# Kernel tuning notes

Measured on AMD Instinct MI355X. Metric: run time of the kernel, lower is better.

The kernel has to match this reference:

```python
import jax, jax.numpy as jnp
import numpy as np

B, T, S, D, V = 8, 128, 400, 512, 50000
EPS_LN = 1e-6

def setup_inputs() -> dict:
    key = jax.random.key(0)
    ks = jax.random.split(key, 10)
    a = jax.random.uniform(ks[0], (B, T, S), dtype=jnp.float32)
    attn_weights = a / jnp.sum(a, axis=-1, keepdims=True)  # row-stochastic like softmax attention
    return {
        'x': jax.random.normal(ks[1], (B, T, D), dtype=jnp.float32),
        'x_t': jax.random.normal(ks[2], (B, T, D), dtype=jnp.float32),
        'memory': jax.random.normal(ks[3], (B, S, D), dtype=jnp.float32),
        'attn_weights': attn_weights,
        'src': jax.random.randint(ks[4], (B, S), 0, V),
        'norm_a': jnp.ones((D,), jnp.float32),
        'norm_b': jnp.zeros((D,), jnp.float32),
        'proj_w': jax.random.normal(ks[5], (V, D), dtype=jnp.float32) * (1.0 / np.sqrt(D)),
        'proj_b': jnp.zeros((V,), jnp.float32),
        'wh_w': jax.random.normal(ks[6], (1, D), dtype=jnp.float32) * (1.0 / np.sqrt(D)),
        'wh_b': jnp.zeros((1,), jnp.float32),
        'ws_w': jax.random.normal(ks[7], (1, D), dtype=jnp.float32) * (1.0 / np.sqrt(D)),
        'ws_b': jnp.zeros((1,), jnp.float32),
        'wx_w': jax.random.normal(ks[8], (1, D), dtype=jnp.float32) * (1.0 / np.sqrt(D)),
        'wx_b': jnp.zeros((1,), jnp.float32),
        'bptr': jnp.zeros((1, 1), jnp.float32),
    }

def _layer_norm(x, a, b):
    mu = jnp.mean(x, axis=-1, keepdims=True)
    sd = jnp.std(x, axis=-1, keepdims=True)
    return a * (x - mu) / (sd + EPS_LN) + b

def reference(x, x_t, memory, attn_weights, src, norm_a, norm_b, proj_w, proj_b,
              wh_w, wh_b, ws_w, ws_b, wx_w, wx_b, bptr):
    # generation distribution over vocab: [B,T,V]
    dec_dist = jnp.einsum('btd,vd->btv', _layer_norm(x, norm_a, norm_b), proj_w) + proj_b
    # context vector h_t = attn @ memory: [B,T,D]
    h_t = jnp.einsum('bts,bsd->btd', attn_weights, memory)
    # p_gen gate: [B,T,1]
    logits = (jnp.einsum('btd,od->bto', h_t, wh_w) + wh_b
              + jnp.einsum('btd,od->bto', x, ws_w) + ws_b
              + jnp.einsum('btd,od->bto', x_t, wx_w) + wx_b
              + bptr[0, 0])
    p_gen = jax.nn.sigmoid(logits)
    # copy distribution via scatter_add of attention mass onto source token ids
    b_idx = jnp.arange(B)[:, None, None]
    t_idx = jnp.arange(T)[None, :, None]
    v_idx = src[:, None, :]  # broadcast over T -> [B,T,S] index
    enc_attn_dist = jnp.zeros((B, T, V), dtype=dec_dist.dtype).at[b_idx, t_idx, v_idx].add(attn_weights)
    out = jnp.log(p_gen * jax.nn.softmax(dec_dist, axis=-1) + (1.0 - p_gen) * enc_attn_dist + 1e-12)
    return out, p_gen
```

## Files before the change

### kernel.cpp

```cpp
#include <hip/hip_runtime.h>
#include <hip/hip_bf16.h>
#include <cstdint>

#define B_  8
#define T_  128
#define S_  400
#define D_  512
#define V_  50000
#define M_  (B_*T_)
#define NT_ 391
#define EPS_LN 1e-6f

#define WCONV_BLKS 12500
#define MW_BLKS    (B_*S_)
#define ROWS_BLKS  M_
#define BM_BLKS    B_
#define BM_WORDS   1600
#define GEMM_BLKS  3128

typedef __bf16 bf16x8 __attribute__((ext_vector_type(8)));
typedef float  f32x4  __attribute__((ext_vector_type(4)));
typedef unsigned short u16;
typedef unsigned short u16x8 __attribute__((ext_vector_type(8)));

__device__ __forceinline__ float bf2f(u16 u) {
    union { unsigned i; float f; } c; c.i = ((unsigned)u) << 16; return c.f;
}
__device__ __forceinline__ u16 f2bf(float f) {
    union { float f; unsigned i; } c; c.f = f;
    unsigned i = c.i;
    unsigned r = (i + 0x7FFFu + ((i >> 16) & 1u)) >> 16;
    return (u16)r;
}

__device__ __forceinline__ float bsum(float v, float* sb) {
    #pragma unroll
    for (int o = 32; o; o >>= 1) v += __shfl_xor(v, o);
    __syncthreads();
    if ((threadIdx.x & 63) == 0) sb[threadIdx.x >> 6] = v;
    __syncthreads();
    return sb[0] + sb[1] + sb[2] + sb[3];
}

__global__ void k_pre(const float* __restrict__ pw, u16* __restrict__ wb,
                      const float* __restrict__ mem, const float* __restrict__ whw,
                      float* __restrict__ mw,
                      const float* __restrict__ x, const float* __restrict__ xt,
                      const float* __restrict__ attn,
                      const float* __restrict__ na, const float* __restrict__ nb,
                      const float* __restrict__ wsw, const float* __restrict__ wxw,
                      const float* __restrict__ whb, const float* __restrict__ wsb,
                      const float* __restrict__ wxb, const float* __restrict__ bp,
                      const int* __restrict__ src, unsigned* __restrict__ bm,
                      int* __restrict__ slot,
                      u16* __restrict__ Ab, float* __restrict__ pgen,
                      float* __restrict__ outp) {
    __shared__ float sb[4];
    __shared__ unsigned sbm[BM_WORDS];
    int bid = blockIdx.x;
    int tid = threadIdx.x;
    if (bid < WCONV_BLKS) {
        size_t i = ((size_t)bid * 256 + tid) * 8;
        float4 a = *(const float4*)(pw + i);
        float4 b = *(const float4*)(pw + i + 4);
        u16x8 o;
        o[0] = f2bf(a.x); o[1] = f2bf(a.y); o[2] = f2bf(a.z); o[3] = f2bf(a.w);
        o[4] = f2bf(b.x); o[5] = f2bf(b.y); o[6] = f2bf(b.z); o[7] = f2bf(b.w);
        *(u16x8*)(wb + i) = o;
        return;
    }
    if (bid < WCONV_BLKS + MW_BLKS) {
        int row = bid - WCONV_BLKS;
        const float* mr = mem + (size_t)row * D_;
        float2 m2 = *(const float2*)(mr + tid * 2);
        float2 w2 = *(const float2*)(whw + tid * 2);
        float tot = bsum(m2.x * w2.x + m2.y * w2.y, sb);
        if (tid == 0) mw[row] = tot;
        return;
    }
    if (bid < WCONV_BLKS + MW_BLKS + ROWS_BLKS) {
        int row = bid - WCONV_BLKS - MW_BLKS;
        int b = row / T_;
        const float* xr  = x  + (size_t)row * D_;
        const float* xtr = xt + (size_t)row * D_;
        float2 xv = *(const float2*)(xr + tid * 2);
        float tsx  = bsum(xv.x + xv.y, sb);
        float tsx2 = bsum(xv.x * xv.x + xv.y * xv.y, sb);
        float mu  = tsx / (float)D_;
        float var = fmaxf(tsx2 / (float)D_ - mu * mu, 0.f);
        float rs  = 1.f / (sqrtf(var) + EPS_LN);
        float2 nav = *(const float2*)(na + tid * 2);
        float2 nbv = *(const float2*)(nb + tid * 2);
        u16 a0 = f2bf(nav.x * (xv.x - mu) * rs + nbv.x);
        u16 a1 = f2bf(nav.y * (xv.y - mu) * rs + nbv.y);
        ((unsigned*)(Ab + (size_t)row * D_))[tid] = (unsigned)a0 | ((unsigned)a1 << 16);
        float2 wsv = *(const float2*)(wsw + tid * 2);
        float2 wxv = *(const float2*)(wxw + tid * 2);
        float2 xtv = *(const float2*)(xtr + tid * 2);
        float dot = xv.x * wsv.x + xv.y * wsv.y + xtv.x * wxv.x + xtv.y * wxv.y;
        if (tid < 200) {
            const float* ar  = attn + (size_t)row * S_;
            const float* mwb = mw + b * S_;
            float2 av = *(const float2*)(ar + tid * 2);
            float2 mv = *(const float2*)(mwb + tid * 2);
            dot += av.x * mv.x + av.y * mv.y;
        }
        float tdot = bsum(dot, sb);
        if (tid == 0) {
            float logit = tdot + whb[0] + wsb[0] + wxb[0] + bp[0];
            float p = 1.f / (1.f + __expf(-logit));
            pgen[row] = p;
            outp[row] = p;
        }
        return;
    }
    {
        int b = bid - WCONV_BLKS - MW_BLKS - ROWS_BLKS;
        for (int i = tid; i < BM_WORDS; i += 256) sbm[i] = 0u;
        const int* sr = src + b * S_;
        int* sl = slot + (size_t)b * V_;
        for (int s = tid; s < S_; s += 256) sl[sr[s]] = 0x7fffffff;
        __syncthreads();
        for (int s = tid; s < S_; s += 256) {
            int v = sr[s];
            atomicOr(&sbm[v >> 5], 1u << (v & 31));
            atomicMin(&sl[v], s);
        }
        __syncthreads();
        unsigned* dst = bm + b * BM_WORDS;
        for (int i = tid; i < BM_WORDS; i += 256) dst[i] = sbm[i];
    }
}

__global__ __launch_bounds__(256) void k_gemm(const u16* __restrict__ Ab,
                                              const u16* __restrict__ Wb,
                                              const float* __restrict__ projb,
                                              u16* __restrict__ dec,
                                              float* __restrict__ psum,
                                              const int* __restrict__ src,
                                              const float* __restrict__ attn,
                                              const int* __restrict__ slot,
                                              float* __restrict__ enc) {
    __shared__ __align__(16) char smem[49152];
    int bid = blockIdx.x;
    int tid = threadIdx.x;
    if (bid >= GEMM_BLKS) {
        int row = bid - GEMM_BLKS;
        int b = row >> 7;
        float* sh_enc = (float*)smem;
        for (int s = tid; s < S_; s += 256) sh_enc[s] = 0.f;
        __syncthreads();
        const int* sr = src + b * S_;
        const int* sl = slot + (size_t)b * V_;
        const float* ar = attn + (size_t)row * S_;
        for (int s = tid; s < S_; s += 256)
            atomicAdd(&sh_enc[sl[sr[s]]], ar[s]);
        __syncthreads();
        float* er = enc + (size_t)row * S_;
        for (int s = tid; s < S_; s += 256) er[s] = sh_enc[s];
        return;
    }
    int xcd = bid & 7, loc = bid >> 3;
    int wg = xcd * NT_ + loc;
    int mt = wg & 7, nt = wg >> 3;
    int brow = mt * 128, bcol = nt * 128;
    int lane = tid & 63, wv = tid >> 6;
    int wm = wv >> 1, wn = wv & 1;
    int kq = lane >> 4, lr = lane & 15;

    size_t aoff[2], boff[2];
    int flatoff[2];
    #pragma unroll
    for (int i = 0; i < 2; ++i) {
        int flat = i * 4096 + tid * 16;
        flatoff[i] = flat;
        int sub = flat >> 10;
        int l   = (flat >> 4) & 63;
        int kq2 = l >> 4, lr2 = l & 15;
        int arow = brow + sub * 16 + lr2;
        int vrow = bcol + sub * 16 + lr2; if (vrow >= V_) vrow = V_ - 1;
        aoff[i] = (size_t)arow * 512 + kq2 * 8;
        boff[i] = (size_t)vrow * 512 + kq2 * 8;
    }

#define STAGE(buf, kt) { \
    char* ab = smem + (buf) * 16384; \
    _Pragma("unroll") \
    for (int i = 0; i < 2; ++i) { \
        __builtin_amdgcn_global_load_lds( \
            (const __attribute__((address_space(1))) unsigned*)(Ab + aoff[i] + (size_t)(kt) * 32), \
            (__attribute__((address_space(3))) unsigned*)(ab + flatoff[i]), 16, 0, 0); \
        __builtin_amdgcn_global_load_lds( \
            (const __attribute__((address_space(1))) unsigned*)(Wb + boff[i] + (size_t)(kt) * 32), \
            (__attribute__((address_space(3))) unsigned*)(ab + 8192 + flatoff[i]), 16, 0, 0); \
    } }

    f32x4 acc[4][4] = {};
    STAGE(0, 0);
    STAGE(1, 1);
    STAGE(2, 2);
    asm volatile("s_waitcnt vmcnt(8)" ::: "memory");
    __builtin_amdgcn_s_barrier();
    __builtin_amdgcn_sched_barrier(0);
    int cur = 0;
    for (int kt = 0; kt < 16; ++kt) {
        const bf16x8* Afp = (const bf16x8*)(smem + cur * 16384);
        const bf16x8* Bfp = (const bf16x8*)(smem + cur * 16384 + 8192);
        bf16x8 af[4], bfr[4];
        #pragma unroll
        for (int m = 0; m < 4; ++m) af[m]  = Afp[(wm * 4 + m) * 64 + lane];
        #pragma unroll
        for (int n = 0; n < 4; ++n) bfr[n] = Bfp[(wn * 4 + n) * 64 + lane];
        #pragma unroll
        for (int m = 0; m < 4; ++m)
            #pragma unroll
            for (int n = 0; n < 4; ++n)
                acc[m][n] = __builtin_amdgcn_mfma_f32_16x16x32_bf16(af[m], bfr[n], acc[m][n], 0, 0, 0);
        __builtin_amdgcn_sched_barrier(0);
        if (kt == 15) break;
        if (kt < 14) { asm volatile("s_waitcnt vmcnt(4)" ::: "memory"); }
        else         { asm volatile("s_waitcnt vmcnt(0)" ::: "memory"); }
        __builtin_amdgcn_s_barrier();
        __builtin_amdgcn_sched_barrier(0);
        if (kt < 13) STAGE(cur, kt + 3);
        cur = (cur == 2) ? 0 : cur + 1;
    }
#undef STAGE
    __syncthreads();

    float pbn[4]; int cvaln[4];
    #pragma unroll
    for (int n = 0; n < 4; ++n) {
        int col = bcol + wn * 64 + n * 16 + lr;
        cvaln[n] = (col < V_);
        pbn[n] = cvaln[n] ? projb[col] : 0.f;
    }
    u16 (*Os)[136] = (u16(*)[136])smem;
    float* ssum = (float*)(smem + 34816);
    #pragma unroll
    for (int m = 0; m < 4; ++m) {
        #pragma unroll
        for (int i = 0; i < 4; ++i) {
            int row128 = wm * 64 + m * 16 + kq * 4 + i;
            float se = 0.f;
            #pragma unroll
            for (int n = 0; n < 4; ++n) {
                float dv = acc[m][n][i] + pbn[n];
                if (cvaln[n]) se += __expf(dv);
                Os[row128][wn * 64 + n * 16 + lr] = f2bf(dv);
            }
            #pragma unroll
            for (int o = 1; o < 16; o <<= 1) se += __shfl_xor(se, o);
            if (lr == 0) ssum[wn * 128 + row128] = se;
        }
    }
    __syncthreads();
    if (tid < 128) {
        psum[(size_t)(brow + tid) * NT_ + nt] = ssum[tid] + ssum[128 + tid];
    }
    #pragma unroll
    for (int j = 0; j < 8; ++j) {
        int row = j * 16 + (tid >> 4);
        int c8 = (tid & 15) * 8;
        int gcol = bcol + c8;
        if (gcol + 8 <= V_) {
            u16x8 v = *(const u16x8*)&Os[row][c8];
            *(u16x8*)(dec + (size_t)(brow + row) * V_ + gcol) = v;
        }
    }
}

__global__ void k_post(const u16* __restrict__ dec, const float* __restrict__ pgen,
                       const float* __restrict__ psum, const unsigned* __restrict__ bm,
                       const int* __restrict__ slot, const float* __restrict__ enc,
                       float* __restrict__ out) {
    __shared__ float sb[4];
    int bid = blockIdx.x;
    int tid = threadIdx.x;
    int c = bid % 25, row = bid / 25;
    int b = row >> 7;
    const float* ps = psum + (size_t)row * NT_;
    float s = 0.f;
    for (int j = tid; j < NT_; j += 256) s += ps[j];
    s = bsum(s, sb);
    float bs = __logf(s);
    float p  = pgen[row];
    float C  = __logf(p) - bs;
    int v0 = c * 2048 + tid * 8;
    if (v0 >= V_) return;
    unsigned w = bm[b * BM_WORDS + (v0 >> 5)];
    unsigned mask = (w >> ((tid & 3) * 8)) & 0xFFu;
    u16x8 d = *(const u16x8*)(dec + (size_t)row * V_ + v0);
    float o[8];
    bool rare = false;
    #pragma unroll
    for (int j = 0; j < 8; ++j) {
        o[j] = bf2f(d[j]) + C;
        rare |= (o[j] < -24.f);
    }
    if (__any(rare)) {
        #pragma unroll
        for (int j = 0; j < 8; ++j)
            if (o[j] < -24.f) o[j] = __logf(__expf(o[j]) + 1e-12f);
    }
    if (mask) {
        const int* sl = slot + (size_t)b * V_;
        const float* er = enc + (size_t)row * S_;
        #pragma unroll
        for (int j = 0; j < 8; ++j) {
            if ((mask >> j) & 1u) {
                float e = er[sl[v0 + j]];
                float dv = bf2f(d[j]);
                o[j] = __logf(p * __expf(dv - bs) + (1.f - p) * e + 1e-12f);
            }
        }
    }
    float* op = out + (size_t)row * V_ + v0;
    float4 o0, o1;
    o0.x = o[0]; o0.y = o[1]; o0.z = o[2]; o0.w = o[3];
    o1.x = o[4]; o1.y = o[5]; o1.z = o[6]; o1.w = o[7];
    *(float4*)op = o0;
    *(float4*)(op + 4) = o1;
}

extern "C" void kernel_launch(void* const* d_in, const int* in_sizes, int n_in,
                              void* d_out, int out_size, void* d_ws, size_t ws_size,
                              hipStream_t stream) {
    const float* x    = (const float*)d_in[0];
    const float* xt   = (const float*)d_in[1];
    const float* mem  = (const float*)d_in[2];
    const float* attn = (const float*)d_in[3];
    const int*   src  = (const int*)d_in[4];
    const float* na   = (const float*)d_in[5];
    const float* nb   = (const float*)d_in[6];
    const float* pw   = (const float*)d_in[7];
    const float* pb   = (const float*)d_in[8];
    const float* whw  = (const float*)d_in[9];
    const float* whb  = (const float*)d_in[10];
    const float* wsw  = (const float*)d_in[11];
    const float* wsb  = (const float*)d_in[12];
    const float* wxw  = (const float*)d_in[13];
    const float* wxb  = (const float*)d_in[14];
    const float* bp   = (const float*)d_in[15];

    char* ws = (char*)d_ws;
    u16*     Wb   = (u16*)(ws + 0);
    u16*     Ab   = (u16*)(ws + 51200000);
    u16*     dec  = (u16*)(ws + 52248576);
    float*   psum = (float*)(ws + 154648576);
    float*   mw   = (float*)(ws + 156250112);
    float*   pgen = (float*)(ws + 156262912);
    unsigned* bmp = (unsigned*)(ws + 156267008);
    int*     slot = (int*)(ws + 156318208);
    float*   enc  = (float*)(ws + 157918208);
    float* out  = (float*)d_out;
    float* outp = out + (size_t)M_ * V_;

    k_pre <<<WCONV_BLKS + MW_BLKS + ROWS_BLKS + BM_BLKS, 256, 0, stream>>>(
              pw, Wb, mem, whw, mw, x, xt, attn, na, nb,
              wsw, wxw, whb, wsb, wxb, bp, src, bmp, slot, Ab, pgen, outp);
    k_gemm<<<GEMM_BLKS + M_, 256, 0, stream>>>(Ab, Wb, pb, dec, psum,
                                               src, attn, slot, enc);
    k_post<<<25 * M_, 256, 0, stream>>>(dec, pgen, psum, bmp, slot, enc, out);
}
```

Baseline: 222.1 us.

## Pre-swizzle GEMM operands into MFMA fragment layout and load directly from global

The bf16 weight conversion and layer-norm output now write their results in a tiled layout that matches the MFMA 16x32 fragment order. This lets the GEMM kernel read each fragment straight from global memory into registers with one contiguous 16-byte load per lane. The LDS triple-buffer pipeline, its barriers and the waitcnt scheduling are removed, and shared memory shrinks to what the epilogue needs. The trade-off is that latency hiding now depends on the fully unrolled loop and on cache hits for the operand reuse that LDS used to provide, since each wave reloads A and B fragments shared with other waves.

```diff
diff --git a/kernel.cpp b/kernel.cpp
--- a/kernel.cpp
+++ b/kernel.cpp
@@ -17,6 +17,7 @@
 #define BM_BLKS    B_
 #define BM_WORDS   1600
 #define GEMM_BLKS  3128
+#define SVMAX      3124
 
 typedef __bf16 bf16x8 __attribute__((ext_vector_type(8)));
 typedef float  f32x4  __attribute__((ext_vector_type(4)));
@@ -41,6 +42,7 @@
     __syncthreads();
     return sb[0] + sb[1] + sb[2] + sb[3];
 }
+
 
 __global__ void k_pre(const float* __restrict__ pw, u16* __restrict__ wb,
                       const float* __restrict__ mem, const float* __restrict__ whw,
@@ -61,12 +63,17 @@
     int tid = threadIdx.x;
     if (bid < WCONV_BLKS) {
         size_t i = ((size_t)bid * 256 + tid) * 8;
+        int v  = (int)(i >> 9);
+        int k0 = (int)(i & 511);
         float4 a = *(const float4*)(pw + i);
         float4 b = *(const float4*)(pw + i + 4);
         u16x8 o;
         o[0] = f2bf(a.x); o[1] = f2bf(a.y); o[2] = f2bf(a.z); o[3] = f2bf(a.w);
         o[4] = f2bf(b.x); o[5] = f2bf(b.y); o[6] = f2bf(b.z); o[7] = f2bf(b.w);
-        *(u16x8*)(wb + i) = o;
+        int sv = v >> 4, ks = k0 >> 5;
+        int l  = ((k0 & 31) >> 3) * 16 + (v & 15);
+        size_t off = (((size_t)sv * 16 + ks) * 64 + l) * 8;
+        *(u16x8*)(wb + off) = o;
         return;
     }
     if (bid < WCONV_BLKS + MW_BLKS) {
@@ -93,7 +100,13 @@
         float2 nbv = *(const float2*)(nb + tid * 2);
         u16 a0 = f2bf(nav.x * (xv.x - mu) * rs + nbv.x);
         u16 a1 = f2bf(nav.y * (xv.y - mu) * rs + nbv.y);
-        ((unsigned*)(Ab + (size_t)row * D_))[tid] = (unsigned)a0 | ((unsigned)a1 << 16);
+        {
+            int k = 2 * tid;
+            int sm = row >> 4, ks = k >> 5;
+            int l  = ((k & 31) >> 3) * 16 + (row & 15);
+            size_t off = (((size_t)sm * 16 + ks) * 64 + l) * 8 + (k & 7);
+            *(unsigned*)(Ab + off) = (unsigned)a0 | ((unsigned)a1 << 16);
+        }
         float2 wsv = *(const float2*)(wsw + tid * 2);
         float2 wxv = *(const float2*)(wxw + tid * 2);
         float2 xtv = *(const float2*)(xtr + tid * 2);
@@ -141,7 +154,7 @@
                                               const float* __restrict__ attn,
                                               const int* __restrict__ slot,
                                               float* __restrict__ enc) {
-    __shared__ __align__(16) char smem[49152];
+    __shared__ __align__(16) char smem[35840];
     int bid = blockIdx.x;
     int tid = threadIdx.x;
     if (bid >= GEMM_BLKS) {
@@ -168,65 +181,35 @@
     int wm = wv >> 1, wn = wv & 1;
     int kq = lane >> 4, lr = lane & 15;
 
-    size_t aoff[2], boff[2];
-    int flatoff[2];
-    #pragma unroll
-    for (int i = 0; i < 2; ++i) {
-        int flat = i * 4096 + tid * 16;
-        flatoff[i] = flat;
-        int sub = flat >> 10;
-        int l   = (flat >> 4) & 63;
-        int kq2 = l >> 4, lr2 = l & 15;
-        int arow = brow + sub * 16 + lr2;
-        int vrow = bcol + sub * 16 + lr2; if (vrow >= V_) vrow = V_ - 1;
-        aoff[i] = (size_t)arow * 512 + kq2 * 8;
-        boff[i] = (size_t)vrow * 512 + kq2 * 8;
-    }
-
-#define STAGE(buf, kt) { \
-    char* ab = smem + (buf) * 16384; \
-    _Pragma("unroll") \
-    for (int i = 0; i < 2; ++i) { \
-        __builtin_amdgcn_global_load_lds( \
-            (const __attribute__((address_space(1))) unsigned*)(Ab + aoff[i] + (size_t)(kt) * 32), \
-            (__attribute__((address_space(3))) unsigned*)(ab + flatoff[i]), 16, 0, 0); \
-        __builtin_amdgcn_global_load_lds( \
-            (const __attribute__((address_space(1))) unsigned*)(Wb + boff[i] + (size_t)(kt) * 32), \
-            (__attribute__((address_space(3))) unsigned*)(ab + 8192 + flatoff[i]), 16, 0, 0); \
-    } }
+    size_t abase[4], bbase[4];
+    #pragma unroll
+    for (int m = 0; m < 4; ++m) {
+        int sm = mt * 8 + wm * 4 + m;
+        abase[m] = (((size_t)sm * 16) * 64 + lane) * 8;
+    }
+    #pragma unroll
+    for (int n = 0; n < 4; ++n) {
+        int sv = nt * 8 + wn * 4 + n;
+        if (sv > SVMAX) sv = SVMAX;
+        bbase[n] = (((size_t)sv * 16) * 64 + lane) * 8;
+    }
 
     f32x4 acc[4][4] = {};
-    STAGE(0, 0);
-    STAGE(1, 1);
-    STAGE(2, 2);
-    asm volatile("s_waitcnt vmcnt(8)" ::: "memory");
-    __builtin_amdgcn_s_barrier();
-    __builtin_amdgcn_sched_barrier(0);
-    int cur = 0;
+    #pragma unroll
     for (int kt = 0; kt < 16; ++kt) {
-        const bf16x8* Afp = (const bf16x8*)(smem + cur * 16384);
-        const bf16x8* Bfp = (const bf16x8*)(smem + cur * 16384 + 8192);
         bf16x8 af[4], bfr[4];
         #pragma unroll
-        for (int m = 0; m < 4; ++m) af[m]  = Afp[(wm * 4 + m) * 64 + lane];
-        #pragma unroll
-        for (int n = 0; n < 4; ++n) bfr[n] = Bfp[(wn * 4 + n) * 64 + lane];
+        for (int m = 0; m < 4; ++m)
+            af[m]  = *(const bf16x8*)(Ab + abase[m] + (size_t)kt * 512);
+        #pragma unroll
+        for (int n = 0; n < 4; ++n)
+            bfr[n] = *(const bf16x8*)(Wb + bbase[n] + (size_t)kt * 512);
         #pragma unroll
         for (int m = 0; m < 4; ++m)
             #pragma unroll
             for (int n = 0; n < 4; ++n)
                 acc[m][n] = __builtin_amdgcn_mfma_f32_16x16x32_bf16(af[m], bfr[n], acc[m][n], 0, 0, 0);
-        __builtin_amdgcn_sched_barrier(0);
-        if (kt == 15) break;
-        if (kt < 14) { asm volatile("s_waitcnt vmcnt(4)" ::: "memory"); }
-        else         { asm volatile("s_waitcnt vmcnt(0)" ::: "memory"); }
-        __builtin_amdgcn_s_barrier();
-        __builtin_amdgcn_sched_barrier(0);
-        if (kt < 13) STAGE(cur, kt + 3);
-        cur = (cur == 2) ? 0 : cur + 1;
-    }
-#undef STAGE
-    __syncthreads();
+    }
 
     float pbn[4]; int cvaln[4];
     #pragma unroll
```

Measured after the change: 247.2 us (median of 2 runs). +11.3%, slower.
